# Performance work log

Hardware: AMD Instinct MI355X
Metric: run time of the kernel (lower is better)

Reference implementation:

```python
import jax, jax.numpy as jnp
import numpy as np

N_NODES = 100000
N_EDGES = 1600000
IN_DIM = 64
EDGE_DIM = 8
H1, H2 = 128, 64
FEAT = 2 * IN_DIM + EDGE_DIM  # 136


def setup_inputs() -> dict:
    key = jax.random.key(0)
    ks = jax.random.split(key, 9)
    z = jax.random.normal(ks[0], (N_NODES, IN_DIM), dtype=jnp.float32)
    edge_index = jax.random.randint(ks[1], (2, N_EDGES), 0, N_NODES, dtype=jnp.int64)
    edge_attr = jax.random.normal(ks[2], (N_EDGES, EDGE_DIM), dtype=jnp.float32)
    # MLP params (Linear stores weight as [out, in]; we keep [in, out] for x @ W)
    def lin(k, fan_in, fan_out):
        bound = 1.0 / np.sqrt(fan_in)
        kw, kb = jax.random.split(k)
        W = jax.random.uniform(kw, (fan_in, fan_out), minval=-bound, maxval=bound, dtype=jnp.float32)
        b = jax.random.uniform(kb, (fan_out,), minval=-bound, maxval=bound, dtype=jnp.float32)
        return W, b
    W1, b1 = lin(ks[3], FEAT, H1)
    W2, b2 = lin(ks[4], H1, H2)
    W3, b3 = lin(ks[5], H2, 1)
    return {"z": z, "edge_index": edge_index, "edge_attr": edge_attr,
            "W1": W1, "b1": b1, "W2": W2, "b2": b2, "W3": W3, "b3": b3}


def reference(z, edge_index, edge_attr, W1, b1, W2, b2, W3, b3):
    src, dst = edge_index[0], edge_index[1]
    # gather node embeddings per edge and concat with edge attributes: [E, 2*D+A]
    feat = jnp.concatenate([z[src], z[dst], edge_attr], axis=-1)
    h = jax.nn.relu(feat @ W1 + b1)   # Dropout is identity in eval mode
    h = jax.nn.relu(h @ W2 + b2)
    logits = (h @ W3 + b3).squeeze(-1)  # [E]
    return logits
```

## Files before the change

### kernel.cpp

```cpp
#include <hip/hip_runtime.h>
#include <hip/hip_bf16.h>
#include <stdint.h>
#include <stddef.h>

#define NODES 100000
#define EDGES 1600000
#define NCHUNK 6250
#define EDGE_GRID 3125
#define NTILES 6250

typedef float f4 __attribute__((ext_vector_type(4)));
typedef float f32x4 __attribute__((ext_vector_type(4)));
typedef short s8v __attribute__((ext_vector_type(8)));
typedef unsigned short u16x8 __attribute__((ext_vector_type(8)));

__device__ __forceinline__ float bf2f(unsigned short u) {
  union { unsigned int i; float f; } v; v.i = ((unsigned int)u) << 16; return v.f;
}
__device__ __forceinline__ unsigned short f2bf(float f) {
  union { float f; unsigned int i; } v; v.f = f;
  return (unsigned short)((v.i + 0x7FFFu + ((v.i >> 16) & 1u)) >> 16);
}
__device__ __forceinline__ short f2bf_hw(float x) {
  __hip_bfloat16 h = __float2bfloat16(x);
  union { __hip_bfloat16 h; short s; } u; u.h = h; return u.s;
}

__global__ __launch_bounds__(256) void node_pq_mfma(
    const float* __restrict__ z, const float* __restrict__ W1,
    const float* __restrict__ b1, unsigned short* __restrict__ PQ) {
  const int t = threadIdx.x;
  const int lane = t & 63;
  const int w = t >> 6;
  const int r = lane & 15, g = lane >> 4;
  const int tile = blockIdx.x * 4 + w;
  if (tile >= NTILES) return;
  const int n0 = tile * 16;

  s8v a_hi[2], a_lo[2];
#pragma unroll
  for (int kt = 0; kt < 2; ++kt) {
    const f4* zp = (const f4*)(z + (size_t)(n0 + r) * 64 + 32 * kt + 8 * g);
    f4 z0 = zp[0], z1 = zp[1];
    float zv[8] = {z0[0], z0[1], z0[2], z0[3], z1[0], z1[1], z1[2], z1[3]};
    s8v hi, lo;
#pragma unroll
    for (int jx = 0; jx < 8; ++jx) {
      short h = f2bf_hw(zv[jx]);
      hi[jx] = h;
      lo[jx] = f2bf_hw(zv[jx] - bf2f((unsigned short)h));
    }
    a_hi[kt] = hi; a_lo[kt] = lo;
  }

#pragma unroll 1
  for (int nt = 0; nt < 16; ++nt) {
    const int col = (nt & 7) * 16 + r;
    const int rowbase = (nt < 8) ? 0 : 64;
    const float init = (nt < 8) ? b1[col] : 0.f;
    f32x4 acc = {init, init, init, init};
#pragma unroll
    for (int kt = 0; kt < 2; ++kt) {
      s8v whi, wlo;
#pragma unroll
      for (int jx = 0; jx < 8; ++jx) {
        float wv = W1[(size_t)(rowbase + 32 * kt + 8 * g + jx) * 128 + col];
        short h = f2bf_hw(wv);
        whi[jx] = h;
        wlo[jx] = f2bf_hw(wv - bf2f((unsigned short)h));
      }
      acc = __builtin_amdgcn_mfma_f32_16x16x32_bf16(a_hi[kt], whi, acc, 0, 0, 0);
      acc = __builtin_amdgcn_mfma_f32_16x16x32_bf16(a_lo[kt], whi, acc, 0, 0, 0);
      acc = __builtin_amdgcn_mfma_f32_16x16x32_bf16(a_hi[kt], wlo, acc, 0, 0, 0);
    }
#pragma unroll
    for (int reg = 0; reg < 4; ++reg)
      PQ[(size_t)(n0 + 4 * g + reg) * 256 + nt * 16 + r] = f2bf(acc[reg]);
  }
}

__global__ __launch_bounds__(256) void edge_mfma_kernel(
    const int* __restrict__ eidx, const float* __restrict__ eattr,
    const float* __restrict__ W1, const float* __restrict__ W2,
    const float* __restrict__ b2, const float* __restrict__ W3,
    const float* __restrict__ b3,
    const unsigned short* __restrict__ PQ, float* __restrict__ out) {
  const int t = threadIdx.x;
  const int lane = t & 63;
  const int w = t >> 6;
  const int r = lane & 15;
  const int g = lane >> 4;

  s8v bfrag[4][4];
#pragma unroll
  for (int kt = 0; kt < 4; ++kt)
#pragma unroll
    for (int nt = 0; nt < 4; ++nt) {
      s8v f;
#pragma unroll
      for (int jx = 0; jx < 8; ++jx) {
        int h = jx >> 2, jp = jx & 3;
        int jjv = 32 * kt + 16 * h + 4 * g + jp;
        f[jx] = (short)f2bf(W2[(size_t)jjv * 64 + nt * 16 + r]);
      }
      bfrag[kt][nt] = f;
    }
  s8v w1cf[8];
#pragma unroll
  for (int mt = 0; mt < 8; ++mt) {
    s8v f = {0, 0, 0, 0, 0, 0, 0, 0};
    if (g == 0) {
#pragma unroll
      for (int jx = 0; jx < 8; ++jx)
        f[jx] = (short)f2bf(W1[(size_t)(128 + jx) * 128 + 16 * mt + r]);
    }
    w1cf[mt] = f;
  }
  s8v a_id = {0, 0, 0, 0, 0, 0, 0, 0};
  if ((g & 1) == (r >> 3)) a_id[r & 7] = (short)0x3F80;

  float b2v[4], w3v[4];
#pragma unroll
  for (int nt = 0; nt < 4; ++nt) { b2v[nt] = b2[nt * 16 + r]; w3v[nt] = W3[nt * 16 + r]; }
  const float bias3 = b3[0];
  const f32x4 zc = {0.f, 0.f, 0.f, 0.f};

#pragma unroll 1
  for (int chunk = blockIdx.x; chunk < NCHUNK; chunk += EDGE_GRID) {
    const int ebase = chunk * 256 + w * 64;
    const int src_all = eidx[ebase + lane];
    const int dst_all = eidx[EDGES + ebase + lane];
    unsigned int ea_pk[4];
    {
      const f4* eap = (const f4*)(eattr + (size_t)(ebase + lane) * 8);
      f4 a0 = eap[0], a1 = eap[1];
      ea_pk[0] = (unsigned int)(unsigned short)f2bf_hw(a0[0]) |
                 ((unsigned int)(unsigned short)f2bf_hw(a0[1]) << 16);
      ea_pk[1] = (unsigned int)(unsigned short)f2bf_hw(a0[2]) |
                 ((unsigned int)(unsigned short)f2bf_hw(a0[3]) << 16);
      ea_pk[2] = (unsigned int)(unsigned short)f2bf_hw(a1[0]) |
                 ((unsigned int)(unsigned short)f2bf_hw(a1[1]) << 16);
      ea_pk[3] = (unsigned int)(unsigned short)f2bf_hw(a1[2]) |
                 ((unsigned int)(unsigned short)f2bf_hw(a1[3]) << 16);
    }

#pragma unroll
    for (int st = 0; st < 4; ++st) {
      const int e0 = ebase + st * 16;
      const int idx = st * 16 + r;
      const int srcv = __shfl(src_all, idx, 64);
      const int dstv = __shfl(dst_all, idx, 64);
      union { unsigned int u[4]; s8v v; } eau;
#pragma unroll
      for (int c = 0; c < 4; ++c) eau.u[c] = (unsigned int)__shfl((int)ea_pk[c], idx, 64);
      const s8v eaf = eau.v;

      const unsigned short* base =
          (g < 2) ? (PQ + (size_t)srcv * 256 + 8 * (g & 1))
                  : (PQ + (size_t)dstv * 256 + 128 + 8 * (g & 1));
      u16x8 bpq[8];
#pragma unroll
      for (int kt = 0; kt < 4; ++kt) {
        bpq[2 * kt]     = *(const u16x8*)(base + 32 * kt);
        bpq[2 * kt + 1] = *(const u16x8*)(base + 32 * kt + 16);
      }

      f32x4 acc[4] = {zc, zc, zc, zc};
#pragma unroll
      for (int kt = 0; kt < 4; ++kt) {
        f32x4 E0 = __builtin_amdgcn_mfma_f32_16x16x32_bf16(w1cf[2 * kt], eaf, zc, 0, 0, 0);
        f32x4 E1 = __builtin_amdgcn_mfma_f32_16x16x32_bf16(w1cf[2 * kt + 1], eaf, zc, 0, 0, 0);
        f32x4 S0 = __builtin_amdgcn_mfma_f32_16x16x32_bf16(a_id, (s8v)bpq[2 * kt], E0, 0, 0, 0);
        f32x4 S1 = __builtin_amdgcn_mfma_f32_16x16x32_bf16(a_id, (s8v)bpq[2 * kt + 1], E1, 0, 0, 0);
        s8v af;
#pragma unroll
        for (int jp = 0; jp < 4; ++jp) {
          af[jp]     = f2bf_hw(fmaxf(S0[jp], 0.f));
          af[4 + jp] = f2bf_hw(fmaxf(S1[jp], 0.f));
        }
#pragma unroll
        for (int nt = 0; nt < 4; ++nt)
          acc[nt] = __builtin_amdgcn_mfma_f32_16x16x32_bf16(af, bfrag[kt][nt], acc[nt], 0, 0, 0);
      }
      float pr0 = 0.f, pr1 = 0.f, pr2 = 0.f, pr3 = 0.f;
#pragma unroll
      for (int nt = 0; nt < 4; ++nt) {
        pr0 = fmaf(fmaxf(acc[nt][0] + b2v[nt], 0.f), w3v[nt], pr0);
        pr1 = fmaf(fmaxf(acc[nt][1] + b2v[nt], 0.f), w3v[nt], pr1);
        pr2 = fmaf(fmaxf(acc[nt][2] + b2v[nt], 0.f), w3v[nt], pr2);
        pr3 = fmaf(fmaxf(acc[nt][3] + b2v[nt], 0.f), w3v[nt], pr3);
      }
#pragma unroll
      for (int m = 1; m < 16; m <<= 1) {
        pr0 += __shfl_xor(pr0, m, 64);
        pr1 += __shfl_xor(pr1, m, 64);
        pr2 += __shfl_xor(pr2, m, 64);
        pr3 += __shfl_xor(pr3, m, 64);
      }
      if (r < 4) {
        float v = (r == 0) ? pr0 : (r == 1) ? pr1 : (r == 2) ? pr2 : pr3;
        out[e0 + 4 * g + r] = v + bias3;
      }
    }
  }
}

extern "C" void kernel_launch(void* const* d_in, const int* in_sizes, int n_in,
                              void* d_out, int out_size, void* d_ws, size_t ws_size,
                              hipStream_t stream) {
  const float* z     = (const float*)d_in[0];
  const int*   eidx  = (const int*)d_in[1];
  const float* eattr = (const float*)d_in[2];
  const float* W1    = (const float*)d_in[3];
  const float* b1    = (const float*)d_in[4];
  const float* W2    = (const float*)d_in[5];
  const float* b2    = (const float*)d_in[6];
  const float* W3    = (const float*)d_in[7];
  const float* b3    = (const float*)d_in[8];
  float* out = (float*)d_out;

  unsigned short* PQ = (unsigned short*)d_ws;
  node_pq_mfma<<<(NTILES + 3) / 4, 256, 0, stream>>>(z, W1, b1, PQ);
  edge_mfma_kernel<<<EDGE_GRID, 256, 0, stream>>>(
      eidx, eattr, W1, W2, b2, W3, b3, PQ, out);
}
```

Baseline: 201.3 us.

## Permute PQ layout and software-pipeline edge gathers, replacing identity-MFMA sum with VALU adds

The node kernel writes P and Q columns in a permuted order so each lane's 8-element gather lines up directly with the MFMA A-fragment layout. The edge kernel then adds P, Q and the edge-attribute term with plain VALU adds instead of the identity-matrix MFMA trick. Gathers for the four sub-tiles are issued ahead of compute (load s+1 before compute s) to hide random-gather latency. The cost is more VGPRs from holding several sub-tiles of gathered data, which may reduce occupancy, plus extra bf16 unpack work on the VALU.

Result: faster. 175.6 us (-12.8%).

```diff
diff --git a/kernel.cpp b/kernel.cpp
--- a/kernel.cpp
+++ b/kernel.cpp
@@ -24,6 +24,10 @@
 __device__ __forceinline__ short f2bf_hw(float x) {
   __hip_bfloat16 h = __float2bfloat16(x);
   union { __hip_bfloat16 h; short s; } u; u.h = h; return u.s;
+}
+
+__device__ __forceinline__ int pqperm(int jj) {
+  return (jj & 0x60) | ((jj & 0x0C) << 1) | ((jj & 0x10) >> 2) | (jj & 3);
 }
 
 __global__ __launch_bounds__(256) void node_pq_mfma(
@@ -73,9 +77,10 @@
       acc = __builtin_amdgcn_mfma_f32_16x16x32_bf16(a_lo[kt], whi, acc, 0, 0, 0);
       acc = __builtin_amdgcn_mfma_f32_16x16x32_bf16(a_hi[kt], wlo, acc, 0, 0, 0);
     }
+    const int outcol = (nt < 8) ? pqperm(col) : (128 + pqperm(col));
 #pragma unroll
     for (int reg = 0; reg < 4; ++reg)
-      PQ[(size_t)(n0 + 4 * g + reg) * 256 + nt * 16 + r] = f2bf(acc[reg]);
+      PQ[(size_t)(n0 + 4 * g + reg) * 256 + outcol] = f2bf(acc[reg]);
   }
 }
 
@@ -116,9 +121,6 @@
     }
     w1cf[mt] = f;
   }
-  s8v a_id = {0, 0, 0, 0, 0, 0, 0, 0};
-  if ((g & 1) == (r >> 3)) a_id[r & 7] = (short)0x3F80;
-
   float b2v[4], w3v[4];
 #pragma unroll
   for (int nt = 0; nt < 4; ++nt) { b2v[nt] = b2[nt * 16 + r]; w3v[nt] = W3[nt * 16 + r]; }
@@ -144,64 +146,82 @@
                  ((unsigned int)(unsigned short)f2bf_hw(a1[3]) << 16);
     }
 
+    int srcv[4], dstv[4];
+    s8v eafv[4];
 #pragma unroll
     for (int st = 0; st < 4; ++st) {
-      const int e0 = ebase + st * 16;
       const int idx = st * 16 + r;
-      const int srcv = __shfl(src_all, idx, 64);
-      const int dstv = __shfl(dst_all, idx, 64);
-      union { unsigned int u[4]; s8v v; } eau;
-#pragma unroll
-      for (int c = 0; c < 4; ++c) eau.u[c] = (unsigned int)__shfl((int)ea_pk[c], idx, 64);
-      const s8v eaf = eau.v;
-
-      const unsigned short* base =
-          (g < 2) ? (PQ + (size_t)srcv * 256 + 8 * (g & 1))
-                  : (PQ + (size_t)dstv * 256 + 128 + 8 * (g & 1));
-      u16x8 bpq[8];
-#pragma unroll
-      for (int kt = 0; kt < 4; ++kt) {
-        bpq[2 * kt]     = *(const u16x8*)(base + 32 * kt);
-        bpq[2 * kt + 1] = *(const u16x8*)(base + 32 * kt + 16);
-      }
-
-      f32x4 acc[4] = {zc, zc, zc, zc};
-#pragma unroll
-      for (int kt = 0; kt < 4; ++kt) {
-        f32x4 E0 = __builtin_amdgcn_mfma_f32_16x16x32_bf16(w1cf[2 * kt], eaf, zc, 0, 0, 0);
-        f32x4 E1 = __builtin_amdgcn_mfma_f32_16x16x32_bf16(w1cf[2 * kt + 1], eaf, zc, 0, 0, 0);
-        f32x4 S0 = __builtin_amdgcn_mfma_f32_16x16x32_bf16(a_id, (s8v)bpq[2 * kt], E0, 0, 0, 0);
-        f32x4 S1 = __builtin_amdgcn_mfma_f32_16x16x32_bf16(a_id, (s8v)bpq[2 * kt + 1], E1, 0, 0, 0);
-        s8v af;
-#pragma unroll
-        for (int jp = 0; jp < 4; ++jp) {
-          af[jp]     = f2bf_hw(fmaxf(S0[jp], 0.f));
-          af[4 + jp] = f2bf_hw(fmaxf(S1[jp], 0.f));
-        }
-#pragma unroll
-        for (int nt = 0; nt < 4; ++nt)
-          acc[nt] = __builtin_amdgcn_mfma_f32_16x16x32_bf16(af, bfrag[kt][nt], acc[nt], 0, 0, 0);
-      }
-      float pr0 = 0.f, pr1 = 0.f, pr2 = 0.f, pr3 = 0.f;
-#pragma unroll
-      for (int nt = 0; nt < 4; ++nt) {
-        pr0 = fmaf(fmaxf(acc[nt][0] + b2v[nt], 0.f), w3v[nt], pr0);
-        pr1 = fmaf(fmaxf(acc[nt][1] + b2v[nt], 0.f), w3v[nt], pr1);
-        pr2 = fmaf(fmaxf(acc[nt][2] + b2v[nt], 0.f), w3v[nt], pr2);
-        pr3 = fmaf(fmaxf(acc[nt][3] + b2v[nt], 0.f), w3v[nt], pr3);
-      }
-#pragma unroll
-      for (int m = 1; m < 16; m <<= 1) {
-        pr0 += __shfl_xor(pr0, m, 64);
-        pr1 += __shfl_xor(pr1, m, 64);
-        pr2 += __shfl_xor(pr2, m, 64);
-        pr3 += __shfl_xor(pr3, m, 64);
-      }
-      if (r < 4) {
-        float v = (r == 0) ? pr0 : (r == 1) ? pr1 : (r == 2) ? pr2 : pr3;
-        out[e0 + 4 * g + r] = v + bias3;
-      }
-    }
+      srcv[st] = __shfl(src_all, idx, 64);
+      dstv[st] = __shfl(dst_all, idx, 64);
+      union { unsigned int u[4]; s8v v; } eu;
+#pragma unroll
+      for (int c = 0; c < 4; ++c) eu.u[c] = (unsigned int)__shfl((int)ea_pk[c], idx, 64);
+      eafv[st] = eu.v;
+    }
+
+    u16x8 p[4][4], q[4][4];
+#define PQ_LOAD(s)                                                             \
+    {                                                                          \
+      const unsigned short* Pb = PQ + (size_t)srcv[s] * 256 + 8 * g;           \
+      const unsigned short* Qb = PQ + (size_t)dstv[s] * 256 + 128 + 8 * g;     \
+      _Pragma("unroll")                                                        \
+      for (int kt = 0; kt < 4; ++kt) {                                         \
+        p[s][kt] = *(const u16x8*)(Pb + 32 * kt);                              \
+        q[s][kt] = *(const u16x8*)(Qb + 32 * kt);                              \
+      }                                                                        \
+    }
+
+#define PQ_COMPUTE(s)                                                          \
+    {                                                                          \
+      const int e0 = ebase + (s) * 16;                                         \
+      f32x4 acc[4] = {zc, zc, zc, zc};                                         \
+      _Pragma("unroll")                                                        \
+      for (int kt = 0; kt < 4; ++kt) {                                         \
+        f32x4 E0 = __builtin_amdgcn_mfma_f32_16x16x32_bf16(w1cf[2 * kt], eafv[s], zc, 0, 0, 0); \
+        f32x4 E1 = __builtin_amdgcn_mfma_f32_16x16x32_bf16(w1cf[2 * kt + 1], eafv[s], zc, 0, 0, 0); \
+        s8v af;                                                                \
+        _Pragma("unroll")                                                      \
+        for (int jp = 0; jp < 4; ++jp) {                                       \
+          float s0 = bf2f(p[s][kt][jp]) + bf2f(q[s][kt][jp]) + E0[jp];         \
+          af[jp] = f2bf_hw(fmaxf(s0, 0.f));                                    \
+          float s1 = bf2f(p[s][kt][4 + jp]) + bf2f(q[s][kt][4 + jp]) + E1[jp]; \
+          af[4 + jp] = f2bf_hw(fmaxf(s1, 0.f));                                \
+        }                                                                      \
+        _Pragma("unroll")                                                      \
+        for (int nt = 0; nt < 4; ++nt)                                         \
+          acc[nt] = __builtin_amdgcn_mfma_f32_16x16x32_bf16(af, bfrag[kt][nt], acc[nt], 0, 0, 0); \
+      }                                                                        \
+      float pr0 = 0.f, pr1 = 0.f, pr2 = 0.f, pr3 = 0.f;                        \
+      _Pragma("unroll")                                                        \
+      for (int nt = 0; nt < 4; ++nt) {                                         \
+        pr0 = fmaf(fmaxf(acc[nt][0] + b2v[nt], 0.f), w3v[nt], pr0);            \
+        pr1 = fmaf(fmaxf(acc[nt][1] + b2v[nt], 0.f), w3v[nt], pr1);            \
+        pr2 = fmaf(fmaxf(acc[nt][2] + b2v[nt], 0.f), w3v[nt], pr2);            \
+        pr3 = fmaf(fmaxf(acc[nt][3] + b2v[nt], 0.f), w3v[nt], pr3);            \
+      }                                                                        \
+      _Pragma("unroll")                                                        \
+      for (int m = 1; m < 16; m <<= 1) {                                       \
+        pr0 += __shfl_xor(pr0, m, 64);                                         \
+        pr1 += __shfl_xor(pr1, m, 64);                                         \
+        pr2 += __shfl_xor(pr2, m, 64);                                         \
+        pr3 += __shfl_xor(pr3, m, 64);                                         \
+      }                                                                        \
+      if (r < 4) {                                                             \
+        float v = (r == 0) ? pr0 : (r == 1) ? pr1 : (r == 2) ? pr2 : pr3;      \
+        out[e0 + 4 * g + r] = v + bias3;                                       \
+      }                                                                        \
+    }
+
+    PQ_LOAD(0)
+    PQ_LOAD(1)
+    PQ_COMPUTE(0)
+    PQ_LOAD(2)
+    PQ_COMPUTE(1)
+    PQ_LOAD(3)
+    PQ_COMPUTE(2)
+    PQ_COMPUTE(3)
+#undef PQ_LOAD
+#undef PQ_COMPUTE
   }
 }
 
```

## Permute PQ layout so edge lanes add P and Q directly, dropping identity MFMAs

Applied to the files above, without the earlier changes.

The node kernel now writes PQ columns in a permuted order that matches the MFMA accumulator layout. Each edge lane can then load its P and Q fragments and add them to the edge-attribute projection in VALU code. This removes the identity-matrix MFMAs that previously did the gather-sum and reduces per-lane gather traffic to contiguous fragments. The edge grid is also shrunk so each block handles more chunks, which trades parallelism for less per-block weight-fragment setup.

After: 173.3 us. -13.9%, faster.

```diff
diff --git a/kernel.cpp b/kernel.cpp
--- a/kernel.cpp
+++ b/kernel.cpp
@@ -6,7 +6,7 @@
 #define NODES 100000
 #define EDGES 1600000
 #define NCHUNK 6250
-#define EDGE_GRID 3125
+#define EDGE_GRID 1250
 #define NTILES 6250
 
 typedef float f4 __attribute__((ext_vector_type(4)));
@@ -24,6 +24,10 @@
 __device__ __forceinline__ short f2bf_hw(float x) {
   __hip_bfloat16 h = __float2bfloat16(x);
   union { __hip_bfloat16 h; short s; } u; u.h = h; return u.s;
+}
+
+__device__ __forceinline__ int pqperm(int jj) {
+  return (jj & 0x60) | ((jj & 0x0C) << 1) | ((jj & 0x10) >> 2) | (jj & 3);
 }
 
 __global__ __launch_bounds__(256) void node_pq_mfma(
@@ -73,9 +77,10 @@
       acc = __builtin_amdgcn_mfma_f32_16x16x32_bf16(a_lo[kt], whi, acc, 0, 0, 0);
       acc = __builtin_amdgcn_mfma_f32_16x16x32_bf16(a_hi[kt], wlo, acc, 0, 0, 0);
     }
+    const int outcol = (nt < 8) ? pqperm(col) : (128 + pqperm(col));
 #pragma unroll
     for (int reg = 0; reg < 4; ++reg)
-      PQ[(size_t)(n0 + 4 * g + reg) * 256 + nt * 16 + r] = f2bf(acc[reg]);
+      PQ[(size_t)(n0 + 4 * g + reg) * 256 + outcol] = f2bf(acc[reg]);
   }
 }
 
@@ -116,9 +121,6 @@
     }
     w1cf[mt] = f;
   }
-  s8v a_id = {0, 0, 0, 0, 0, 0, 0, 0};
-  if ((g & 1) == (r >> 3)) a_id[r & 7] = (short)0x3F80;
-
   float b2v[4], w3v[4];
 #pragma unroll
   for (int nt = 0; nt < 4; ++nt) { b2v[nt] = b2[nt * 16 + r]; w3v[nt] = W3[nt * 16 + r]; }
@@ -150,33 +152,33 @@
       const int idx = st * 16 + r;
       const int srcv = __shfl(src_all, idx, 64);
       const int dstv = __shfl(dst_all, idx, 64);
-      union { unsigned int u[4]; s8v v; } eau;
-#pragma unroll
-      for (int c = 0; c < 4; ++c) eau.u[c] = (unsigned int)__shfl((int)ea_pk[c], idx, 64);
-      const s8v eaf = eau.v;
-
-      const unsigned short* base =
-          (g < 2) ? (PQ + (size_t)srcv * 256 + 8 * (g & 1))
-                  : (PQ + (size_t)dstv * 256 + 128 + 8 * (g & 1));
-      u16x8 bpq[8];
+      s8v eaf;
+#pragma unroll
+      for (int c = 0; c < 4; ++c) {
+        unsigned int pk = (unsigned int)__shfl((int)ea_pk[c], idx, 64);
+        eaf[2 * c] = (short)(pk & 0xFFFFu);
+        eaf[2 * c + 1] = (short)(pk >> 16);
+      }
+      const unsigned short* Pb = PQ + (size_t)srcv * 256 + 8 * g;
+      const unsigned short* Qb = PQ + (size_t)dstv * 256 + 128 + 8 * g;
+      u16x8 p[4], q[4];
 #pragma unroll
       for (int kt = 0; kt < 4; ++kt) {
-        bpq[2 * kt]     = *(const u16x8*)(base + 32 * kt);
-        bpq[2 * kt + 1] = *(const u16x8*)(base + 32 * kt + 16);
-      }
-
+        p[kt] = *(const u16x8*)(Pb + 32 * kt);
+        q[kt] = *(const u16x8*)(Qb + 32 * kt);
+      }
       f32x4 acc[4] = {zc, zc, zc, zc};
 #pragma unroll
       for (int kt = 0; kt < 4; ++kt) {
         f32x4 E0 = __builtin_amdgcn_mfma_f32_16x16x32_bf16(w1cf[2 * kt], eaf, zc, 0, 0, 0);
         f32x4 E1 = __builtin_amdgcn_mfma_f32_16x16x32_bf16(w1cf[2 * kt + 1], eaf, zc, 0, 0, 0);
-        f32x4 S0 = __builtin_amdgcn_mfma_f32_16x16x32_bf16(a_id, (s8v)bpq[2 * kt], E0, 0, 0, 0);
-        f32x4 S1 = __builtin_amdgcn_mfma_f32_16x16x32_bf16(a_id, (s8v)bpq[2 * kt + 1], E1, 0, 0, 0);
         s8v af;
 #pragma unroll
         for (int jp = 0; jp < 4; ++jp) {
-          af[jp]     = f2bf_hw(fmaxf(S0[jp], 0.f));
-          af[4 + jp] = f2bf_hw(fmaxf(S1[jp], 0.f));
+          float s0 = bf2f(p[kt][jp]) + bf2f(q[kt][jp]) + E0[jp];
+          af[jp] = f2bf_hw(fmaxf(s0, 0.f));
+          float s1 = bf2f(p[kt][4 + jp]) + bf2f(q[kt][4 + jp]) + E1[jp];
+          af[4 + jp] = f2bf_hw(fmaxf(s1, 0.f));
         }
 #pragma unroll
         for (int nt = 0; nt < 4; ++nt)
```
